# Optimization experiments

Hardware: AMD Instinct MI355X
Metric: run time of the kernel (lower is better)

## Reference

```python
import jax, jax.numpy as jnp
import numpy as np
import math

DIM = 256
PATCH = 16  # Patchnum
H = W = 64  # feature_size
B = 16


def _conv(x, w, pad):
    # x: [B,C,H,W], w: [O,I,kh,kw]
    return jax.lax.conv_general_dilated(
        x, w, window_strides=(1, 1), padding=[(pad, pad), (pad, pad)],
        dimension_numbers=('NCHW', 'OIHW', 'NCHW'))


def setup_inputs() -> dict:
    key = jax.random.key(0)
    ks = jax.random.split(key, 6)
    fan = DIM * 9
    s3 = 1.0 / math.sqrt(fan)
    s1 = 1.0 / math.sqrt(DIM)
    return {
        'e': jax.random.normal(ks[0], (B, DIM, H, W), dtype=jnp.float32),
        'pam_out': jax.random.normal(ks[1], (B, DIM, PATCH, PATCH), dtype=jnp.float32),
        'q_w': jax.random.uniform(ks[2], (DIM, DIM, 3, 3), jnp.float32, -s3, s3),
        'k_w': jax.random.uniform(ks[3], (DIM, DIM, 3, 3), jnp.float32, -s3, s3),
        'v_w': jax.random.uniform(ks[4], (DIM, DIM, 3, 3), jnp.float32, -s3, s3),
        'proj_w': jax.random.uniform(ks[5], (DIM, DIM, 1, 1), jnp.float32, -s1, s1),
    }


def reference(e, pam_out, q_w, k_w, v_w, proj_w):
    b, c, h, w = e.shape
    # AdaptiveAvgPool2d((PATCH, PATCH)) with h % PATCH == 0 -> mean pooling
    fh, fw = h // PATCH, w // PATCH
    max_e = e.reshape(b, c, PATCH, fh, PATCH, fw).mean(axis=(3, 5))
    q = _conv(max_e, q_w, 1).reshape(b, c, PATCH * PATCH)      # [b,c,P^2]
    k = _conv(pam_out, k_w, 1).reshape(b, c, PATCH * PATCH)    # [b,c,P^2]
    v = _conv(e, v_w, 1).reshape(b, c, h * w)                  # [b,c,HW]
    # L2 normalize along token dim (torch F.normalize, eps=1e-12)
    q = q / jnp.maximum(jnp.linalg.norm(q, axis=-1, keepdims=True), 1e-12)
    k = k / jnp.maximum(jnp.linalg.norm(k, axis=-1, keepdims=True), 1e-12)
    attn = jnp.einsum('bcn,bdn->bcd', q, k) / math.sqrt(c)     # [b,c,c]
    attn = jax.nn.softmax(attn, axis=-1)
    out = jnp.einsum('bcd,bdn->bcn', attn, v).reshape(b, c, h, w)
    out = _conv(out, proj_w, 0) + e
    return out
```

## Files before the change

### kernel.cpp

```cpp
#include <hip/hip_runtime.h>
#include <hip/hip_bf16.h>

#define NB 16
#define NC 256
#define NPIX 4096

typedef __attribute__((ext_vector_type(8))) short short8;
typedef __attribute__((ext_vector_type(4))) short short4v;
typedef __attribute__((ext_vector_type(4))) float f32x4;

static __device__ __forceinline__ ushort f2bf(float f) {
    __hip_bfloat16 h = __float2bfloat16(f);
    return *(ushort*)&h;
}

static __device__ __forceinline__ void gload_lds16(const ushort* g, ushort* l) {
    __builtin_amdgcn_global_load_lds(
        (const __attribute__((address_space(1))) unsigned int*)g,
        (__attribute__((address_space(3))) unsigned int*)l, 16, 0, 0);
}

__global__ void __launch_bounds__(256) prep_k(
    const float* __restrict__ e, const float* __restrict__ pam,
    const float* __restrict__ qw, const float* __restrict__ kw,
    const float* __restrict__ vw, const float* __restrict__ pw,
    ushort* __restrict__ maxeT, ushort* __restrict__ pamT,
    ushort* __restrict__ wqT, ushort* __restrict__ wkT,
    ushort* __restrict__ pbf, ushort* __restrict__ vwT,
    float* __restrict__ qnorm, float* __restrict__ knorm) {
    __shared__ float smem[9216];
    int blk = blockIdx.x, t = threadIdx.x;
    if (blk < 1024) {
        int b = blk >> 6, c0 = (blk & 63) * 4;
        int py = t >> 4, px4 = (t & 15) * 4;
        float s[4];
#pragma unroll
        for (int cc = 0; cc < 4; ++cc) {
            const float* p = e + (size_t)(b * 256 + c0 + cc) * NPIX;
            float a = 0.f;
#pragma unroll
            for (int r = 0; r < 4; ++r) {
                float4 v = *(const float4*)(p + (py * 4 + r) * 64 + px4);
                a += v.x + v.y + v.z + v.w;
            }
            s[cc] = a * 0.0625f;
        }
        short4v v;
#pragma unroll
        for (int cc = 0; cc < 4; ++cc) v[cc] = (short)f2bf(s[cc]);
        *(short4v*)(maxeT + (size_t)b * 65536 + (size_t)t * 256 + c0) = v;
    } else if (blk < 1280) {
        int bb = blk - 1024;
        int b = bb >> 4, cg = bb & 15;
        float (*lt)[256] = (float(*)[256])smem;
#pragma unroll
        for (int cc = 0; cc < 16; ++cc)
            lt[cc][t] = pam[(size_t)(b * 256 + cg * 16 + cc) * 256 + t];
        __syncthreads();
        ushort* dstb = pamT + (size_t)b * 65536 + (size_t)t * 256 + cg * 16;
#pragma unroll
        for (int g = 0; g < 2; ++g) {
            short8 v;
#pragma unroll
            for (int k = 0; k < 8; ++k) v[k] = (short)f2bf(lt[g * 8 + k][t]);
            *(short8*)(dstb + g * 8) = v;
        }
    } else if (blk < 1792) {
        int idx = blk - 1280;
        const float* src = (idx < 256) ? qw : kw;
        ushort* dst = (idx < 256) ? wqT : wkT;
        int o = idx & 255;
        float wv[9];
#pragma unroll
        for (int j = 0; j < 9; ++j) wv[j] = src[(size_t)o * 2304 + t * 9 + j];
#pragma unroll
        for (int j = 0; j < 9; ++j) dst[(size_t)j * 65536 + (size_t)o * 256 + t] = f2bf(wv[j]);
    } else if (blk < 1808) {
        int base = (blk - 1792) * 4096;
        for (int g = 0; g < 16; ++g) {
            int idx = base + g * 256 + t;
            pbf[idx] = f2bf(pw[idx]);
        }
    } else if (blk < 1872) {
        int d0 = (blk - 1808) * 4;
        float* lt = smem;
        for (int u = 0; u < 36; ++u) lt[u * 256 + t] = vw[(size_t)d0 * 2304 + u * 256 + t];
        __syncthreads();
#pragma unroll
        for (int r = 0; r < 9; ++r) {
            int idx = r * 256 + t;
            int i = idx / 9, j = idx % 9;
            short4v v;
#pragma unroll
            for (int dd = 0; dd < 4; ++dd) v[dd] = (short)f2bf(lt[dd * 2304 + idx]);
            *(short4v*)(vwT + ((size_t)(j * 256 + i)) * 256 + d0) = v;
        }
    } else {
        for (int g = 0; g < 16; ++g) {
            qnorm[g * 256 + t] = 0.f;
            knorm[g * 256 + t] = 0.f;
        }
    }
}

__global__ void __launch_bounds__(256, 2) conv16_mfma(const ushort* __restrict__ maxeT,
                                                      const ushort* __restrict__ pamT,
                                                      const ushort* __restrict__ wqT,
                                                      const ushort* __restrict__ wkT,
                                                      ushort* __restrict__ qb,
                                                      ushort* __restrict__ kTb,
                                                      float* __restrict__ qnorm,
                                                      float* __restrict__ knorm) {
    int blk = blockIdx.x;
    int qk = blk >> 8;
    int b  = (blk >> 4) & 15;
    int og = (blk >> 2) & 3;
    int tg = blk & 3;
    const ushort* inT = qk ? pamT : maxeT;
    const ushort* wt  = qk ? wkT : wqT;
    ushort* outp      = qk ? kTb : qb;
    float* nrm        = qk ? knorm : qnorm;
    int tid = threadIdx.x, wid = tid >> 6, lane = tid & 63;
    int wm = wid >> 1, wn = wid & 1;
    int kq = lane >> 4, l16 = lane & 15;
    int ty0 = tg * 4;
    __shared__ ushort Bs[96][256];
    __shared__ ushort As[2][64][64];
    const ushort* itb = inT + (size_t)b * 65536;
    {
#pragma unroll
        for (int j = 0; j < 12; ++j) {
            int d = (j * 4 + wid) * 64 + lane;
            int tok = d >> 5, u = d & 31;
            int lr = tok >> 4, tx = tok & 15;
            int gy = min(max(ty0 - 1 + lr, 0), 15);
            gload_lds16(itb + (gy * 16 + tx) * 256 + ((u ^ (tok & 7)) * 8),
                        &Bs[0][0] + (size_t)(j * 4 + wid) * 512);
        }
    }
    int aoff[2];
#pragma unroll
    for (int j = 0; j < 2; ++j) {
        int d = (j * 4 + wid) * 64 + lane;
        int o = d >> 3, u = d & 7;
        aoff[j] = (og * 64 + o) * 256 + ((u ^ (o & 7)) * 8);
    }
    auto stageA = [&](int s, int buf) {
        const ushort* base = wt + (size_t)(s >> 2) * 65536 + (s & 3) * 64;
#pragma unroll
        for (int j = 0; j < 2; ++j)
            gload_lds16(base + aoff[j], &As[buf][0][0] + (size_t)(j * 4 + wid) * 512);
    };
    stageA(0, 0);
    stageA(1, 1);
    __syncthreads();
    f32x4 acc[2][2];
#pragma unroll
    for (int mf = 0; mf < 2; ++mf)
#pragma unroll
        for (int nf = 0; nf < 2; ++nf) acc[mf][nf] = (f32x4){0.f, 0.f, 0.f, 0.f};
    const short8 zf = {};
    for (int s = 0; s < 36; ++s) {
        int tap = s >> 2, kh = s & 3;
        int dy = tap / 3 - 1, dx = tap % 3 - 1;
        const ushort* bp[2]; bool ok[2]; int lt7[2];
#pragma unroll
        for (int nf = 0; nf < 2; ++nf) {
            int n = tg * 64 + wn * 32 + nf * 16 + l16;
            int ny = (n >> 4) + dy, nx = (n & 15) + dx;
            ok[nf] = ((unsigned)ny < 16u) && ((unsigned)nx < 16u);
            int lrc = min(max(ny - ty0 + 1, 0), 5);
            int nxc = min(max(nx, 0), 15);
            int ltok = lrc * 16 + nxc;
            bp[nf] = &Bs[ltok][0];
            lt7[nf] = ltok & 7;
        }
#pragma unroll
        for (int kc = 0; kc < 2; ++kc) {
            int ua = kc * 4 + kq;
            int ub = kh * 8 + kc * 4 + kq;
            short8 af[2], bfr[2];
#pragma unroll
            for (int mf = 0; mf < 2; ++mf) {
                int o = wm * 32 + mf * 16 + l16;
                af[mf] = *(const short8*)(&As[s & 1][o][(ua ^ (o & 7)) * 8]);
            }
#pragma unroll
            for (int nf = 0; nf < 2; ++nf) {
                short8 v = *(const short8*)(bp[nf] + ((ub ^ lt7[nf]) * 8));
                bfr[nf] = ok[nf] ? v : zf;
            }
#pragma unroll
            for (int mf = 0; mf < 2; ++mf)
#pragma unroll
                for (int nf = 0; nf < 2; ++nf)
                    acc[mf][nf] = __builtin_amdgcn_mfma_f32_16x16x32_bf16(af[mf], bfr[nf], acc[mf][nf], 0, 0, 0);
        }
        __syncthreads();
        if (s + 2 < 36) stageA(s + 2, s & 1);
    }
    float ss[2][4];
#pragma unroll
    for (int mf = 0; mf < 2; ++mf)
#pragma unroll
        for (int r = 0; r < 4; ++r) ss[mf][r] = 0.f;
#pragma unroll
    for (int mf = 0; mf < 2; ++mf)
#pragma unroll
        for (int nf = 0; nf < 2; ++nf)
#pragma unroll
            for (int r = 0; r < 4; ++r) ss[mf][r] += acc[mf][nf][r] * acc[mf][nf][r];
#pragma unroll
    for (int mf = 0; mf < 2; ++mf)
#pragma unroll
        for (int r = 0; r < 4; ++r) {
#pragma unroll
            for (int off = 1; off < 16; off <<= 1) ss[mf][r] += __shfl_xor(ss[mf][r], off, 64);
        }
    if (l16 == 0) {
#pragma unroll
        for (int mf = 0; mf < 2; ++mf)
#pragma unroll
            for (int r = 0; r < 4; ++r)
                atomicAdd(&nrm[b * 256 + og * 64 + wm * 32 + mf * 16 + kq * 4 + r], ss[mf][r]);
    }
    ushort* ob = outp + (size_t)b * 65536;
#pragma unroll
    for (int mf = 0; mf < 2; ++mf)
#pragma unroll
        for (int nf = 0; nf < 2; ++nf) {
            int col = tg * 64 + wn * 32 + nf * 16 + l16;
#pragma unroll
            for (int r = 0; r < 4; ++r) {
                int row = og * 64 + wm * 32 + mf * 16 + kq * 4 + r;
                ob[(size_t)row * 256 + col] = f2bf(acc[mf][nf][r]);
            }
        }
}

__global__ void __launch_bounds__(512) attn_mfma(const ushort* __restrict__ qb,
                                                 const ushort* __restrict__ kTb,
                                                 const float* __restrict__ qnorm,
                                                 const float* __restrict__ knorm,
                                                 ushort* __restrict__ attnT) {
    int blk = blockIdx.x;
    int b = (blk & 7) + 8 * ((blk >> 3) & 1);
    int cg = blk >> 4;
    int tid = threadIdx.x, wid = tid >> 6, lane = tid & 63;
    int rw = wid & 3, chf = wid >> 2;
    int kq = lane >> 4, l16 = lane & 15;
    int c0w = cg * 64 + rw * 16;
    int lrow = rw * 16 + kq * 4;
    f32x4 acc[8];
#pragma unroll
    for (int nf = 0; nf < 8; ++nf) acc[nf] = (f32x4){0.f, 0.f, 0.f, 0.f};
    const ushort* qp = qb + (size_t)b * 65536;
    const ushort* kp = kTb + (size_t)b * 65536 + (size_t)(chf * 128) * 256;
    for (int kc = 0; kc < 8; ++kc) {
        short8 af = *(const short8*)(qp + (size_t)(c0w + l16) * 256 + kc * 32 + kq * 8);
#pragma unroll
        for (int nf = 0; nf < 8; ++nf) {
            short8 bf = *(const short8*)(kp + (size_t)(nf * 16 + l16) * 256 + kc * 32 + kq * 8);
            acc[nf] = __builtin_amdgcn_mfma_f32_16x16x32_bf16(af, bf, acc[nf], 0, 0, 0);
        }
    }
    float rq[4], rk[8];
#pragma unroll
    for (int r = 0; r < 4; ++r)
        rq[r] = rsqrtf(fmaxf(qnorm[b * 256 + c0w + kq * 4 + r], 1e-24f)) * 0.0625f;
#pragma unroll
    for (int nf = 0; nf < 8; ++nf)
        rk[nf] = rsqrtf(fmaxf(knorm[b * 256 + chf * 128 + nf * 16 + l16], 1e-24f));
#pragma unroll
    for (int nf = 0; nf < 8; ++nf)
#pragma unroll
        for (int r = 0; r < 4; ++r) acc[nf][r] *= rq[r] * rk[nf];
    __shared__ float red[64][2];
    float m4[4], s4[4];
#pragma unroll
    for (int r = 0; r < 4; ++r) {
        float m = -1e30f;
#pragma unroll
        for (int nf = 0; nf < 8; ++nf) m = fmaxf(m, acc[nf][r]);
#pragma unroll
        for (int off = 1; off < 16; off <<= 1) m = fmaxf(m, __shfl_xor(m, off, 64));
        m4[r] = m;
    }
    if (l16 == 0) {
#pragma unroll
        for (int r = 0; r < 4; ++r) red[lrow + r][chf] = m4[r];
    }
    __syncthreads();
#pragma unroll
    for (int r = 0; r < 4; ++r) m4[r] = fmaxf(red[lrow + r][0], red[lrow + r][1]);
    __syncthreads();
#pragma unroll
    for (int r = 0; r < 4; ++r) {
        float s = 0.f;
#pragma unroll
        for (int nf = 0; nf < 8; ++nf) {
            float ex = __expf(acc[nf][r] - m4[r]);
            acc[nf][r] = ex;
            s += ex;
        }
#pragma unroll
        for (int off = 1; off < 16; off <<= 1) s += __shfl_xor(s, off, 64);
        s4[r] = s;
    }
    if (l16 == 0) {
#pragma unroll
        for (int r = 0; r < 4; ++r) red[lrow + r][chf] = s4[r];
    }
    __syncthreads();
#pragma unroll
    for (int r = 0; r < 4; ++r) {
        float inv = 1.0f / (red[lrow + r][0] + red[lrow + r][1]);
#pragma unroll
        for (int nf = 0; nf < 8; ++nf) acc[nf][r] *= inv;
    }
    ushort* ap = attnT + (size_t)b * 65536;
#pragma unroll
    for (int nf = 0; nf < 8; ++nf) {
        int d = chf * 128 + nf * 16 + l16;
        short4v v;
#pragma unroll
        for (int r = 0; r < 4; ++r) v[r] = (short)f2bf(acc[nf][r]);
        *(short4v*)(ap + (size_t)d * 256 + c0w + kq * 4) = v;
    }
}

__global__ void __launch_bounds__(512) mproj_mfma(const ushort* __restrict__ pbf,
                                                  const ushort* __restrict__ attnT,
                                                  ushort* __restrict__ Mbf) {
    int blk = blockIdx.x;
    int b = (blk & 7) + 8 * ((blk >> 3) & 1);
    int og = blk >> 4;
    int tid = threadIdx.x, wid = tid >> 6, lane = tid & 63;
    int rw = wid & 3, chf = wid >> 2;
    int kq = lane >> 4, l16 = lane & 15;
    int o0w = og * 64 + rw * 16;
    f32x4 acc[8];
#pragma unroll
    for (int nf = 0; nf < 8; ++nf) acc[nf] = (f32x4){0.f, 0.f, 0.f, 0.f};
    const ushort* ap = attnT + (size_t)b * 65536 + (size_t)(chf * 128) * 256;
    for (int kc = 0; kc < 8; ++kc) {
        short8 af = *(const short8*)(pbf + (size_t)(o0w + l16) * 256 + kc * 32 + kq * 8);
#pragma unroll
        for (int nf = 0; nf < 8; ++nf) {
            short8 bf = *(const short8*)(ap + (size_t)(nf * 16 + l16) * 256 + kc * 32 + kq * 8);
            acc[nf] = __builtin_amdgcn_mfma_f32_16x16x32_bf16(af, bf, acc[nf], 0, 0, 0);
        }
    }
    ushort* mb = Mbf + (size_t)b * 65536;
#pragma unroll
    for (int nf = 0; nf < 8; ++nf)
#pragma unroll
        for (int r = 0; r < 4; ++r)
            mb[(size_t)(o0w + kq * 4 + r) * 256 + chf * 128 + nf * 16 + l16] = f2bf(acc[nf][r]);
}

__global__ void __launch_bounds__(512) weff_mfma(const ushort* __restrict__ Mbf,
                                                 const ushort* __restrict__ vwT,
                                                 ushort* __restrict__ wbf) {
    int blk = blockIdx.x;
    int i = blk >> 3;
    int b = (blk & 7) + 8 * (i >> 4);
    int j = i & 15;
    if (j >= 9) return;
    int tid = threadIdx.x;
    int wid = tid >> 6, lane = tid & 63;
    int wm = wid >> 1, wn = wid & 1;
    int kq = lane >> 4, l16 = lane & 15;
    f32x4 acc[4][8];
#pragma unroll
    for (int mf = 0; mf < 4; ++mf)
#pragma unroll
        for (int nf = 0; nf < 8; ++nf) acc[mf][nf] = (f32x4){0.f, 0.f, 0.f, 0.f};
    const ushort* abase = Mbf + (size_t)b * 65536 + (size_t)(wm * 64 + l16) * 256 + kq * 8;
    const ushort* bbase = vwT + (size_t)(j * 256 + wn * 128 + l16) * 256 + kq * 8;
    for (int kc = 0; kc < 8; ++kc) {
        int d0 = kc * 32;
        short8 af[4], bfr[8];
#pragma unroll
        for (int mf = 0; mf < 4; ++mf) af[mf] = *(const short8*)(abase + mf * 16 * 256 + d0);
#pragma unroll
        for (int nf = 0; nf < 8; ++nf) bfr[nf] = *(const short8*)(bbase + nf * 16 * 256 + d0);
#pragma unroll
        for (int mf = 0; mf < 4; ++mf)
#pragma unroll
            for (int nf = 0; nf < 8; ++nf)
                acc[mf][nf] = __builtin_amdgcn_mfma_f32_16x16x32_bf16(af[mf], bfr[nf], acc[mf][nf], 0, 0, 0);
    }
    ushort* wout = wbf + ((size_t)(b * 9 + j)) * 65536;
#pragma unroll
    for (int mf = 0; mf < 4; ++mf) {
        int o = wm * 64 + mf * 16 + kq * 4;
#pragma unroll
        for (int nf = 0; nf < 8; ++nf) {
            int ic = wn * 128 + nf * 16 + l16;
#pragma unroll
            for (int r = 0; r < 4; ++r)
                wout[(size_t)(o + r) * 256 + ic] = f2bf(acc[mf][nf][r]);
        }
    }
}

__global__ void __launch_bounds__(512, 4) bigconv_mfma(const float* __restrict__ e,
                                                       const ushort* __restrict__ wbf,
                                                       float* __restrict__ out) {
    int blk = blockIdx.x;
    int ibf = blk >> 3;
    int b = (blk & 7) + 8 * (ibf >> 5);
    int rem = ibf & 31;
    int pt = rem >> 1, oh = rem & 1;
    int y0 = pt * 4;
    int tid = threadIdx.x, wid = tid >> 6, lane = tid & 63;
    int wr = wid >> 1, wo = wid & 1;
    int kq = lane >> 4, l16 = lane & 15;
    __shared__ ushort Bs[6][64][64];
    __shared__ ushort As[2][128][64];
    f32x4 acc[4][4];
#pragma unroll
    for (int mf = 0; mf < 4; ++mf)
#pragma unroll
        for (int nf = 0; nf < 4; ++nf) acc[mf][nf] = (f32x4){0.f, 0.f, 0.f, 0.f};
    const float* eb = e + (size_t)b * NC * NPIX;
    const ushort* wb = wbf + (size_t)b * 589824;
    const short8 zf = {};
    int c2 = tid & 31, rr = tid >> 5;
    int sr = rr >> 1, sq = rr & 1;
    bool bstage = (rr < 12);
    int syc = min(max(y0 - 1 + sr, 0), 63);
    int ao[2], asd[2];
#pragma unroll
    for (int j = 0; j < 2; ++j) {
        int du = (j * 8 + wid) * 64 + lane;
        ao[j] = du >> 3;
        asd[j] = (lane & 7) ^ (ao[j] & 7);
    }

    for (int ci = 0; ci < 4; ++ci) {
        __syncthreads();
        if (bstage) {
            const float* s0 = eb + ((size_t)(ci * 64 + 2 * c2) * 64 + syc) * 64 + sq * 32;
            const float* s1 = s0 + NPIX;
            uint* bsrow = (uint*)&Bs[sr][0][0];
#pragma unroll
            for (int h = 0; h < 2; ++h) {
                float4 va[4], vb[4];
#pragma unroll
                for (int q = 0; q < 4; ++q) va[q] = *(const float4*)(s0 + h * 16 + q * 4);
#pragma unroll
                for (int q = 0; q < 4; ++q) vb[q] = *(const float4*)(s1 + h * 16 + q * 4);
#pragma unroll
                for (int q = 0; q < 4; ++q) {
#pragma unroll
                    for (int m2 = 0; m2 < 4; ++m2) {
                        int px = sq * 32 + h * 16 + q * 4 + m2;
                        float f0 = ((const float*)&va[q])[m2];
                        float f1 = ((const float*)&vb[q])[m2];
                        uint pk = (uint)f2bf(f0) | ((uint)f2bf(f1) << 16);
                        int s = (c2 >> 2) ^ (px & 7);
                        bsrow[px * 32 + s * 4 + (c2 & 3)] = pk;
                    }
                }
            }
        }
        {
#pragma unroll
            for (int j = 0; j < 2; ++j) {
                const ushort* src = wb + (size_t)(oh * 128 + ao[j]) * 256 + ci * 64 + asd[j] * 8;
                gload_lds16(src, &As[0][0][0] + (size_t)(j * 8 + wid) * 512);
            }
        }
        __syncthreads();
        int cur = 0;
        for (int tap = 0; tap < 9; ++tap) {
            if (tap < 8) {
#pragma unroll
                for (int j = 0; j < 2; ++j) {
                    const ushort* src = wb + (size_t)(tap + 1) * 65536 +
                                        (size_t)(oh * 128 + ao[j]) * 256 + ci * 64 + asd[j] * 8;
                    gload_lds16(src, &As[cur ^ 1][0][0] + (size_t)(j * 8 + wid) * 512);
                }
            }
            {
                int dy = tap / 3 - 1, dx = tap % 3 - 1;
                int rl = wr + dy + 1;
                bool rowok = (unsigned)(y0 + wr + dy) < 64u;
                const ushort* bp[4]; bool ok[4]; int p7[4];
#pragma unroll
                for (int nf = 0; nf < 4; ++nf) {
                    int pxr = nf * 16 + l16 + dx;
                    ok[nf] = rowok && ((unsigned)pxr < 64u);
                    int pxc = min(max(pxr, 0), 63);
                    bp[nf] = &Bs[rl][pxc][0];
                    p7[nf] = pxc & 7;
                }
#pragma unroll
                for (int kc = 0; kc < 2; ++kc) {
                    int sd = kc * 4 + kq;
                    short8 af[4];
#pragma unroll
                    for (int mf = 0; mf < 4; ++mf) {
                        int o = wo * 64 + mf * 16 + l16;
                        af[mf] = *(const short8*)(&As[cur][o][(sd ^ (o & 7)) * 8]);
                    }
                    short8 bfr[4];
#pragma unroll
                    for (int nf = 0; nf < 4; ++nf) {
                        short8 v = *(const short8*)(bp[nf] + (sd ^ p7[nf]) * 8);
                        bfr[nf] = ok[nf] ? v : zf;
                    }
#pragma unroll
                    for (int mf = 0; mf < 4; ++mf)
#pragma unroll
                        for (int nf = 0; nf < 4; ++nf)
                            acc[mf][nf] = __builtin_amdgcn_mfma_f32_16x16x32_bf16(af[mf], bfr[nf], acc[mf][nf], 0, 0, 0);
                }
            }
            __syncthreads();
            cur ^= 1;
        }
    }
    int prow = y0 + wr;
    float* ob = out + (size_t)b * NC * NPIX;
#pragma unroll
    for (int mf = 0; mf < 4; ++mf) {
        int o = oh * 128 + wo * 64 + mf * 16 + kq * 4;
#pragma unroll
        for (int nf = 0; nf < 4; ++nf) {
            int p = prow * 64 + nf * 16 + l16;
#pragma unroll
            for (int r = 0; r < 4; ++r) {
                size_t idx = (size_t)(o + r) * NPIX + p;
                ob[idx] = acc[mf][nf][r] + eb[idx];
            }
        }
    }
}

extern "C" void kernel_launch(void* const* d_in, const int* in_sizes, int n_in,
                              void* d_out, int out_size, void* d_ws, size_t ws_size,
                              hipStream_t stream) {
    const float* e   = (const float*)d_in[0];
    const float* pam = (const float*)d_in[1];
    const float* qw  = (const float*)d_in[2];
    const float* kw  = (const float*)d_in[3];
    const float* vw  = (const float*)d_in[4];
    const float* pw  = (const float*)d_in[5];
    float* out = (float*)d_out;
    float* ws  = (float*)d_ws;

    ushort* wbf  = (ushort*)ws;
    float*  S    = ws + 4718592;
    ushort* maxeT = (ushort*)S;
    ushort* pamT  = (ushort*)(S + 524288);
    ushort* wqT   = (ushort*)(S + 1048576);
    ushort* wkT   = (ushort*)(S + 1343488);
    ushort* pbf   = (ushort*)(S + 1638400);
    ushort* vwT   = (ushort*)(S + 1671168);
    float*  qnorm = S + 1966080;
    float*  knorm = S + 1970176;
    ushort* qb    = (ushort*)ws;
    ushort* kTb   = (ushort*)(ws + 524288);
    ushort* attnT = maxeT;
    ushort* Mbf   = pamT;

    prep_k<<<1873, 256, 0, stream>>>(e, pam, qw, kw, vw, pw,
                                     maxeT, pamT, wqT, wkT, pbf, vwT, qnorm, knorm);
    conv16_mfma<<<512, 256, 0, stream>>>(maxeT, pamT, wqT, wkT, qb, kTb, qnorm, knorm);
    attn_mfma<<<64, 512, 0, stream>>>(qb, kTb, qnorm, knorm, attnT);
    mproj_mfma<<<64, 512, 0, stream>>>(pbf, attnT, Mbf);
    weff_mfma<<<256, 512, 0, stream>>>(Mbf, vwT, wbf);
    bigconv_mfma<<<512, 512, 0, stream>>>(e, wbf, out);
}
```

Before: 204.4 us.

## Compute all output channels per block in bigconv and prefetch weights two taps ahead

The fused 3x3 conv kernel now has each block cover all 256 output channels for a 4-row strip, instead of splitting the channels across two blocks. This halves the redundant fp32-to-bf16 staging of the input e and doubles the reuse of each B fragment across MFMAs. The grid shrinks to 256 blocks with a larger weight tile in LDS and a 4x8 accumulator tile per wave. Weight staging is rearranged to prefetch two taps ahead into the double buffer, and a barrier at the start of the channel loop is dropped. The cost is more registers and LDS per block, lower occupancy, and only one block per CU to hide latency.

After: 210.8 us. +3.1%, slower.

```diff
diff --git a/kernel.cpp b/kernel.cpp
--- a/kernel.cpp
+++ b/kernel.cpp
@@ -405,25 +405,23 @@
     }
 }
 
-__global__ void __launch_bounds__(512, 4) bigconv_mfma(const float* __restrict__ e,
+__global__ void __launch_bounds__(512, 2) bigconv_mfma(const float* __restrict__ e,
                                                        const ushort* __restrict__ wbf,
                                                        float* __restrict__ out) {
     int blk = blockIdx.x;
-    int ibf = blk >> 3;
-    int b = (blk & 7) + 8 * (ibf >> 5);
-    int rem = ibf & 31;
-    int pt = rem >> 1, oh = rem & 1;
+    int b = (blk & 7) + 8 * (blk >> 7);
+    int pt = (blk >> 3) & 15;
     int y0 = pt * 4;
     int tid = threadIdx.x, wid = tid >> 6, lane = tid & 63;
-    int wr = wid >> 1, wo = wid & 1;
+    int wy = wid >> 2, wo = wid & 3;
     int kq = lane >> 4, l16 = lane & 15;
     __shared__ ushort Bs[6][64][64];
-    __shared__ ushort As[2][128][64];
-    f32x4 acc[4][4];
+    __shared__ ushort As[2][256][64];
+    f32x4 acc[4][8];
 #pragma unroll
     for (int mf = 0; mf < 4; ++mf)
 #pragma unroll
-        for (int nf = 0; nf < 4; ++nf) acc[mf][nf] = (f32x4){0.f, 0.f, 0.f, 0.f};
+        for (int nf = 0; nf < 8; ++nf) acc[mf][nf] = (f32x4){0.f, 0.f, 0.f, 0.f};
     const float* eb = e + (size_t)b * NC * NPIX;
     const ushort* wb = wbf + (size_t)b * 589824;
     const short8 zf = {};
@@ -431,16 +429,22 @@
     int sr = rr >> 1, sq = rr & 1;
     bool bstage = (rr < 12);
     int syc = min(max(y0 - 1 + sr, 0), 63);
-    int ao[2], asd[2];
-#pragma unroll
-    for (int j = 0; j < 2; ++j) {
+    int ao[4], asd[4];
+#pragma unroll
+    for (int j = 0; j < 4; ++j) {
         int du = (j * 8 + wid) * 64 + lane;
         ao[j] = du >> 3;
-        asd[j] = (lane & 7) ^ (ao[j] & 7);
-    }
+        asd[j] = (du & 7) ^ (ao[j] & 7);
+    }
+    auto stageA = [&](int tap, int buf, int ci) {
+        const ushort* base = wb + (size_t)tap * 65536 + ci * 64;
+#pragma unroll
+        for (int j = 0; j < 4; ++j)
+            gload_lds16(base + (size_t)ao[j] * 256 + asd[j] * 8,
+                        &As[buf][0][0] + (size_t)(j * 8 + wid) * 512);
+    };
 
     for (int ci = 0; ci < 4; ++ci) {
-        __syncthreads();
         if (bstage) {
             const float* s0 = eb + ((size_t)(ci * 64 + 2 * c2) * 64 + syc) * 64 + sq * 32;
             const float* s1 = s0 + NPIX;
@@ -466,33 +470,21 @@
                 }
             }
         }
-        {
-#pragma unroll
-            for (int j = 0; j < 2; ++j) {
-                const ushort* src = wb + (size_t)(oh * 128 + ao[j]) * 256 + ci * 64 + asd[j] * 8;
-                gload_lds16(src, &As[0][0][0] + (size_t)(j * 8 + wid) * 512);
-            }
-        }
+        stageA(0, 0, ci);
+        stageA(1, 1, ci);
         __syncthreads();
-        int cur = 0;
         for (int tap = 0; tap < 9; ++tap) {
-            if (tap < 8) {
-#pragma unroll
-                for (int j = 0; j < 2; ++j) {
-                    const ushort* src = wb + (size_t)(tap + 1) * 65536 +
-                                        (size_t)(oh * 128 + ao[j]) * 256 + ci * 64 + asd[j] * 8;
-                    gload_lds16(src, &As[cur ^ 1][0][0] + (size_t)(j * 8 + wid) * 512);
-                }
-            }
+            int cur = tap & 1;
             {
                 int dy = tap / 3 - 1, dx = tap % 3 - 1;
-                int rl = wr + dy + 1;
-                bool rowok = (unsigned)(y0 + wr + dy) < 64u;
-                const ushort* bp[4]; bool ok[4]; int p7[4];
-#pragma unroll
-                for (int nf = 0; nf < 4; ++nf) {
-                    int pxr = nf * 16 + l16 + dx;
-                    ok[nf] = rowok && ((unsigned)pxr < 64u);
+                const ushort* bp[8]; bool ok[8]; int p7[8];
+#pragma unroll
+                for (int nf = 0; nf < 8; ++nf) {
+                    int h = nf >> 2;
+                    int yabs = y0 + wy * 2 + h + dy;
+                    int rl = wy * 2 + h + dy + 1;
+                    int pxr = (nf & 3) * 16 + l16 + dx;
+                    ok[nf] = ((unsigned)yabs < 64u) && ((unsigned)pxr < 64u);
                     int pxc = min(max(pxr, 0), 63);
                     bp[nf] = &Bs[rl][pxc][0];
                     p7[nf] = pxc & 7;
@@ -506,31 +498,31 @@
                         int o = wo * 64 + mf * 16 + l16;
                         af[mf] = *(const short8*)(&As[cur][o][(sd ^ (o & 7)) * 8]);
                     }
-                    short8 bfr[4];
-#pragma unroll
-                    for (int nf = 0; nf < 4; ++nf) {
+                    short8 bfr[8];
+#pragma unroll
+                    for (int nf = 0; nf < 8; ++nf) {
                         short8 v = *(const short8*)(bp[nf] + (sd ^ p7[nf]) * 8);
                         bfr[nf] = ok[nf] ? v : zf;
                     }
 #pragma unroll
                     for (int mf = 0; mf < 4; ++mf)
 #pragma unroll
-                        for (int nf = 0; nf < 4; ++nf)
+                        for (int nf = 0; nf < 8; ++nf)
                             acc[mf][nf] = __builtin_amdgcn_mfma_f32_16x16x32_bf16(af[mf], bfr[nf], acc[mf][nf], 0, 0, 0);
                 }
             }
             __syncthreads();
-            cur ^= 1;
-        }
-    }
-    int prow = y0 + wr;
+            if (tap + 2 < 9) stageA(tap + 2, cur, ci);
+        }
+    }
     float* ob = out + (size_t)b * NC * NPIX;
 #pragma unroll
     for (int mf = 0; mf < 4; ++mf) {
-        int o = oh * 128 + wo * 64 + mf * 16 + kq * 4;
-#pragma unroll
-        for (int nf = 0; nf < 4; ++nf) {
-            int p = prow * 64 + nf * 16 + l16;
+        int o = wo * 64 + mf * 16 + kq * 4;
+#pragma unroll
+        for (int nf = 0; nf < 8; ++nf) {
+            int y = y0 + wy * 2 + (nf >> 2);
+            int p = y * 64 + (nf & 3) * 16 + l16;
 #pragma unroll
             for (int r = 0; r < 4; ++r) {
                 size_t idx = (size_t)(o + r) * NPIX + p;
@@ -573,5 +565,5 @@
     attn_mfma<<<64, 512, 0, stream>>>(qb, kTb, qnorm, knorm, attnT);
     mproj_mfma<<<64, 512, 0, stream>>>(pbf, attnT, Mbf);
     weff_mfma<<<256, 512, 0, stream>>>(Mbf, vwT, wbf);
-    bigconv_mfma<<<512, 512, 0, stream>>>(e, wbf, out);
-}
+    bigconv_mfma<<<256, 512, 0, stream>>>(e, wbf, out);
+}
```
